# Kernel tuning notes

Hardware: AMD Instinct MI355X
Metric: run time of the kernel (lower is better)

The kernel has to match this reference:

```python
import jax, jax.numpy as jnp
import numpy as np

B, T, Q, K, H = 8, 128, 64, 64, 4  # batch, agents, q_dim, kv_dim, heads; neighbors n = T-1


def setup_inputs() -> dict:
    key = jax.random.key(0)
    ks = jax.random.split(key, 9)
    s = 0.05
    return {
        "q_x": jax.random.normal(ks[0], (B, T, Q), dtype=jnp.float32),
        "kv_x": jax.random.normal(ks[1], (B, T, T - 1, K), dtype=jnp.float32),
        # nn.Linear weights stored (out_features, in_features), y = x @ W.T + b
        "Wk": jax.random.normal(ks[2], (H * K, K), dtype=jnp.float32) * s,      # tokeys (no bias)
        "Wq": jax.random.normal(ks[3], (H * K, Q), dtype=jnp.float32) * s,      # toqueries (no bias)
        "Wv": jax.random.normal(ks[4], (H * K, K + Q), dtype=jnp.float32) * s,  # tovalues
        "bv": jax.random.normal(ks[5], (H * K,), dtype=jnp.float32) * s,
        "bias": jax.random.uniform(ks[6], (K,), dtype=jnp.float32, minval=-0.1, maxval=0.1),
        "ws": jax.random.normal(ks[7], (K,), dtype=jnp.float32) * s,            # score_proj weight (1, K) -> (K,)
        "bs": jax.random.normal(ks[8], (), dtype=jnp.float32) * s,              # score_proj bias
    }


def reference(q_x, kv_x, Wk, Wq, Wv, bv, bias, ws, bs):
    b, t, n, k = kv_x.shape            # n = t - 1 neighbors
    q = q_x.shape[-1]
    h = Wk.shape[0] // k
    # key / query projections
    keys = jnp.einsum('btnk,ok->btno', kv_x, Wk).reshape(b, t, n, h, k)
    queries = jnp.einsum('btq,oq->bto', q_x, Wq).reshape(b, t, 1, h, k)
    # additive (Bahdanau) score: linear(tanh(keys + queries + bias)) -> scalar per (b,t,n,h)
    score = jnp.einsum('btnhk,k->btnh', jnp.tanh(keys + queries + bias), ws) + bs
    # values from concat(kv, broadcast query features)
    q_exp = jnp.broadcast_to(q_x[:, :, None, :], (b, t, n, q))
    value_input = jnp.concatenate([kv_x, q_exp], axis=-1)      # (b,t,n,k+q)
    values = (jnp.einsum('btnc,oc->btno', value_input, Wv) + bv).reshape(b, t, n, h, k)
    # softmax over neighbors, weighted sum of values
    w = jax.nn.softmax(score, axis=2)                          # (b,t,n,h)
    x = jnp.einsum('btnh,btnhk->bthk', w, values).reshape(b, t, h * k)
    return x
```

## Files before the change

kernel.cpp:

```cpp
#include <hip/hip_runtime.h>
#include <hip/hip_bf16.h>

#define NB 127
#define SCALE 2.885390081777927f

typedef __attribute__((ext_vector_type(8))) short bf16x8;
typedef __attribute__((ext_vector_type(4))) float f32x4;

#define WKP_S  0
#define WVP_S  16384
#define WQP_S  32768
#define WVQP_S 49152
#define WS_NEEDED ((size_t)(4 * 16384 * 2))

__device__ __forceinline__ short bfs(float f) {
  __hip_bfloat16 h = __float2bfloat16(f);
  return __builtin_bit_cast(short, h);
}
__device__ __forceinline__ unsigned packbf2(float a, float b) {
  unsigned lo = (unsigned short)bfs(a);
  unsigned hi = (unsigned short)bfs(b);
  return lo | (hi << 16);
}
__device__ __forceinline__ bf16x8 gath_s(const float* __restrict__ p, float s) {
  float4 a = *(const float4*)p;
  float4 b = *(const float4*)(p + 4);
  bf16x8 f;
  f[0] = bfs(a.x * s); f[1] = bfs(a.y * s); f[2] = bfs(a.z * s); f[3] = bfs(a.w * s);
  f[4] = bfs(b.x * s); f[5] = bfs(b.y * s); f[6] = bfs(b.z * s); f[7] = bfs(b.w * s);
  return f;
}

__global__ __launch_bounds__(256, 2) void
pack_kernel(const float* __restrict__ Wk, const float* __restrict__ Wq,
            const float* __restrict__ Wv, short* __restrict__ dstall)
{
  const int blk = blockIdx.x;
  const int tid = threadIdx.x;
  const int m = blk >> 4, sub = blk & 15;
  const float* src; int stride, off, dsto; float scl;
  if (m == 0)      { src = Wk; stride = 64;  off = 0;  dsto = WKP_S;  scl = SCALE; }
  else if (m == 1) { src = Wv; stride = 128; off = 0;  dsto = WVP_S;  scl = 1.f; }
  else if (m == 2) { src = Wq; stride = 64;  off = 0;  dsto = WQP_S;  scl = SCALE; }
  else             { src = Wv; stride = 128; off = 64; dsto = WVQP_S; scl = 1.f; }
  short* dst = dstall + dsto;
  int i4 = sub * 256 + tid;
  int o = i4 >> 4, c4 = i4 & 15;
  float4 v = ((const float4*)(src + o * stride + off))[c4];
  int k0 = c4 * 4;
  int kt = k0 >> 5, gg = (k0 & 31) >> 3, j0 = k0 & 7;
  int head = o >> 6, nt = (o >> 4) & 3, ol = o & 15;
  int di = ((((head * 4 + nt) * 2 + kt) * 64) + gg * 16 + ol) * 8 + j0;
  *(uint2*)(dst + di) = make_uint2(packbf2(v.x * scl, v.y * scl),
                                   packbf2(v.z * scl, v.w * scl));
}

template <int PREP>
__global__ __launch_bounds__(256, 4) void
rnn_attn_kernel(const float* __restrict__ q_x, const float* __restrict__ kv_x,
                const float* __restrict__ Wk, const float* __restrict__ Wq,
                const float* __restrict__ Wv, const float* __restrict__ bv,
                const float* __restrict__ bias, const float* __restrict__ wsc,
                const short* __restrict__ pack, float* __restrict__ out)
{
  __shared__ __align__(16) unsigned char Atile[128 * 128];
  __shared__ float scs[4][128];
  __shared__ float4 qv_lds[4][4][4];

  const int tid = threadIdx.x;
  const int bt = blockIdx.x;
  const int lane = tid & 63;
  const int head = tid >> 6;
  const int l15 = lane & 15;
  const int g = lane >> 4;

  const float* kv = kv_x + (size_t)bt * (NB * 64);
  #pragma unroll
  for (int i = 0; i < 8; ++i) {
    int idx = i * 256 + tid;
    int row = idx >> 4, c = idx & 15;
    float4 v = (row < NB) ? ((const float4*)kv)[idx] : make_float4(0.f, 0.f, 0.f, 0.f);
    int byte = (row << 7) + (c << 3);
    byte ^= ((row & 7) << 4);
    *(uint2*)(&Atile[byte]) = make_uint2(packbf2(v.x, v.y), packbf2(v.z, v.w));
  }

  f32x4 qq[4];
  {
    bf16x8 qf0 = gath_s(q_x + bt * 64 + g * 8, 1.f);
    bf16x8 qf1 = gath_s(q_x + bt * 64 + 32 + g * 8, 1.f);
    #pragma unroll
    for (int nt = 0; nt < 4; ++nt) {
      bf16x8 wv0, wv1;
      if (PREP) {
        const bf16x8* pv = (const bf16x8*)(pack + WVQP_S);
        wv0 = pv[((head * 4 + nt) * 2 + 0) * 64 + lane];
        wv1 = pv[((head * 4 + nt) * 2 + 1) * 64 + lane];
      } else {
        int o = head * 64 + nt * 16 + l15;
        wv0 = gath_s(Wv + o * 128 + 64 + g * 8, 1.f);
        wv1 = gath_s(Wv + o * 128 + 64 + 32 + g * 8, 1.f);
      }
      float4 bv4 = ((const float4*)(bv + head * 64))[nt * 4 + g];
      f32x4 b = (f32x4){bv4.x, bv4.y, bv4.z, bv4.w};
      b = __builtin_amdgcn_mfma_f32_16x16x32_bf16(wv0, qf0, b, 0, 0, 0);
      b = __builtin_amdgcn_mfma_f32_16x16x32_bf16(wv1, qf1, b, 0, 0, 0);
      if (l15 == 0) qv_lds[head][nt][g] = make_float4(b[0], b[1], b[2], b[3]);
    }
    #pragma unroll
    for (int nt = 0; nt < 4; ++nt) {
      bf16x8 wq0, wq1;
      if (PREP) {
        const bf16x8* pw = (const bf16x8*)(pack + WQP_S);
        wq0 = pw[((head * 4 + nt) * 2 + 0) * 64 + lane];
        wq1 = pw[((head * 4 + nt) * 2 + 1) * 64 + lane];
      } else {
        int o = head * 64 + nt * 16 + l15;
        wq0 = gath_s(Wq + o * 64 + g * 8, SCALE);
        wq1 = gath_s(Wq + o * 64 + 32 + g * 8, SCALE);
      }
      float4 bs4 = ((const float4*)bias)[nt * 4 + g];
      f32x4 a = (f32x4){bs4.x * SCALE, bs4.y * SCALE, bs4.z * SCALE, bs4.w * SCALE};
      a = __builtin_amdgcn_mfma_f32_16x16x32_bf16(wq0, qf0, a, 0, 0, 0);
      a = __builtin_amdgcn_mfma_f32_16x16x32_bf16(wq1, qf1, a, 0, 0, 0);
      qq[nt] = a;
    }
  }

  __syncthreads();

  #pragma unroll
  for (int h = 0; h < 2; ++h) {
    bf16x8 b00, b01, b10, b11;
    if (PREP) {
      const bf16x8* pw = (const bf16x8*)(pack + WKP_S);
      b00 = pw[((head * 4 + 2 * h + 0) * 2 + 0) * 64 + lane];
      b01 = pw[((head * 4 + 2 * h + 0) * 2 + 1) * 64 + lane];
      b10 = pw[((head * 4 + 2 * h + 1) * 2 + 0) * 64 + lane];
      b11 = pw[((head * 4 + 2 * h + 1) * 2 + 1) * 64 + lane];
    } else {
      int o0 = head * 64 + (2 * h) * 16 + l15;
      b00 = gath_s(Wk + o0 * 64 + g * 8, SCALE);
      b01 = gath_s(Wk + o0 * 64 + 32 + g * 8, SCALE);
      b10 = gath_s(Wk + (o0 + 16) * 64 + g * 8, SCALE);
      b11 = gath_s(Wk + (o0 + 16) * 64 + 32 + g * 8, SCALE);
    }
    float4 ta = ((const float4*)wsc)[(2 * h) * 4 + g];
    float4 tb = ((const float4*)wsc)[(2 * h + 1) * 4 + g];
    f32x4 wsa = (f32x4){-2.f * ta.x, -2.f * ta.y, -2.f * ta.z, -2.f * ta.w};
    f32x4 wsb = (f32x4){-2.f * tb.x, -2.f * tb.y, -2.f * tb.z, -2.f * tb.w};
    f32x4 qa = qq[2 * h], qb = qq[2 * h + 1];

    #pragma unroll 1
    for (int mt = 0; mt < 8; ++mt) {
      int row = mt * 16 + l15;
      int byte0 = (row << 7) + g * 16;
      int swz = (l15 & 7) << 4;
      bf16x8 a0 = *(const bf16x8*)(&Atile[byte0 ^ swz]);
      bf16x8 a1 = *(const bf16x8*)(&Atile[(byte0 + 64) ^ swz]);
      float p = 0.f;
      f32x4 acc = qa;
      acc = __builtin_amdgcn_mfma_f32_16x16x32_bf16(b00, a0, acc, 0, 0, 0);
      acc = __builtin_amdgcn_mfma_f32_16x16x32_bf16(b01, a1, acc, 0, 0, 0);
      #pragma unroll
      for (int r = 0; r < 4; ++r)
        p = fmaf(wsa[r], __builtin_amdgcn_rcpf(__builtin_amdgcn_exp2f(acc[r]) + 1.f), p);
      f32x4 acc2 = qb;
      acc2 = __builtin_amdgcn_mfma_f32_16x16x32_bf16(b10, a0, acc2, 0, 0, 0);
      acc2 = __builtin_amdgcn_mfma_f32_16x16x32_bf16(b11, a1, acc2, 0, 0, 0);
      #pragma unroll
      for (int r = 0; r < 4; ++r)
        p = fmaf(wsb[r], __builtin_amdgcn_rcpf(__builtin_amdgcn_exp2f(acc2[r]) + 1.f), p);
      p += __shfl_xor(p, 16);
      p += __shfl_xor(p, 32);
      if (g == 0) {
        int idx = mt * 16 + l15;
        scs[head][idx] = h ? (scs[head][idx] + p) : p;
      }
    }
  }

  {
    float s0 = scs[head][l15 + 0],  s1 = scs[head][l15 + 16];
    float s2 = scs[head][l15 + 32], s3 = scs[head][l15 + 48];
    float s4 = scs[head][l15 + 64], s5 = scs[head][l15 + 80];
    float s6 = scs[head][l15 + 96], s7 = scs[head][l15 + 112];
    if (l15 == 15) s7 = -3.0e38f;
    float m = fmaxf(fmaxf(fmaxf(s0, s1), fmaxf(s2, s3)),
                    fmaxf(fmaxf(s4, s5), fmaxf(s6, s7)));
    #pragma unroll
    for (int d = 1; d < 16; d <<= 1) m = fmaxf(m, __shfl_xor(m, d));
    float e0 = __expf(s0 - m), e1 = __expf(s1 - m), e2 = __expf(s2 - m), e3 = __expf(s3 - m);
    float e4 = __expf(s4 - m), e5 = __expf(s5 - m), e6 = __expf(s6 - m), e7 = __expf(s7 - m);
    float sum = ((e0 + e1) + (e2 + e3)) + ((e4 + e5) + (e6 + e7));
    #pragma unroll
    for (int d = 1; d < 16; d <<= 1) sum += __shfl_xor(sum, d);
    float inv = __builtin_amdgcn_rcpf(sum);
    if (g == 0) {
      scs[head][l15 + 0]  = e0 * inv; scs[head][l15 + 16] = e1 * inv;
      scs[head][l15 + 32] = e2 * inv; scs[head][l15 + 48] = e3 * inv;
      scs[head][l15 + 64] = e4 * inv; scs[head][l15 + 80] = e5 * inv;
      scs[head][l15 + 96] = e6 * inv; scs[head][l15 + 112] = e7 * inv;
    }
  }

  #pragma unroll
  for (int h = 0; h < 2; ++h) {
    bf16x8 w00, w01, w10, w11;
    if (PREP) {
      const bf16x8* pw = (const bf16x8*)(pack + WVP_S);
      w00 = pw[((head * 4 + 2 * h + 0) * 2 + 0) * 64 + lane];
      w01 = pw[((head * 4 + 2 * h + 0) * 2 + 1) * 64 + lane];
      w10 = pw[((head * 4 + 2 * h + 1) * 2 + 0) * 64 + lane];
      w11 = pw[((head * 4 + 2 * h + 1) * 2 + 1) * 64 + lane];
    } else {
      int o0 = head * 64 + (2 * h) * 16 + l15;
      w00 = gath_s(Wv + o0 * 128 + g * 8, 1.f);
      w01 = gath_s(Wv + o0 * 128 + 32 + g * 8, 1.f);
      w10 = gath_s(Wv + (o0 + 16) * 128 + g * 8, 1.f);
      w11 = gath_s(Wv + (o0 + 16) * 128 + 32 + g * 8, 1.f);
    }
    f32x4 c0 = (f32x4){0.f, 0.f, 0.f, 0.f};
    f32x4 c1 = (f32x4){0.f, 0.f, 0.f, 0.f};
    #pragma unroll 1
    for (int mt = 0; mt < 8; ++mt) {
      int row = mt * 16 + l15;
      int byte0 = (row << 7) + g * 16;
      int swz = (l15 & 7) << 4;
      bf16x8 a0 = *(const bf16x8*)(&Atile[byte0 ^ swz]);
      bf16x8 a1 = *(const bf16x8*)(&Atile[(byte0 + 64) ^ swz]);
      float w = scs[head][mt * 16 + l15];
      f32x4 v = (f32x4){0.f, 0.f, 0.f, 0.f};
      v = __builtin_amdgcn_mfma_f32_16x16x32_bf16(w00, a0, v, 0, 0, 0);
      v = __builtin_amdgcn_mfma_f32_16x16x32_bf16(w01, a1, v, 0, 0, 0);
      #pragma unroll
      for (int r = 0; r < 4; ++r) c0[r] = fmaf(v[r], w, c0[r]);
      f32x4 v2 = (f32x4){0.f, 0.f, 0.f, 0.f};
      v2 = __builtin_amdgcn_mfma_f32_16x16x32_bf16(w10, a0, v2, 0, 0, 0);
      v2 = __builtin_amdgcn_mfma_f32_16x16x32_bf16(w11, a1, v2, 0, 0, 0);
      #pragma unroll
      for (int r = 0; r < 4; ++r) c1[r] = fmaf(v2[r], w, c1[r]);
    }
    #pragma unroll
    for (int d = 1; d < 16; d <<= 1) {
      #pragma unroll
      for (int r = 0; r < 4; ++r) {
        c0[r] += __shfl_xor(c0[r], d);
        c1[r] += __shfl_xor(c1[r], d);
      }
    }
    if (l15 == 0) {
      float4 qv4 = qv_lds[head][2 * h][g];
      float4 o4 = make_float4(c0[0] + qv4.x, c0[1] + qv4.y, c0[2] + qv4.z, c0[3] + qv4.w);
      ((float4*)out)[bt * 64 + head * 16 + (2 * h) * 4 + g] = o4;
      float4 qv5 = qv_lds[head][2 * h + 1][g];
      float4 o5 = make_float4(c1[0] + qv5.x, c1[1] + qv5.y, c1[2] + qv5.z, c1[3] + qv5.w);
      ((float4*)out)[bt * 64 + head * 16 + (2 * h + 1) * 4 + g] = o5;
    }
  }
}

extern "C" void kernel_launch(void* const* d_in, const int* in_sizes, int n_in,
                              void* d_out, int out_size, void* d_ws, size_t ws_size,
                              hipStream_t stream) {
  const float* q_x  = (const float*)d_in[0];
  const float* kv_x = (const float*)d_in[1];
  const float* Wk   = (const float*)d_in[2];
  const float* Wq   = (const float*)d_in[3];
  const float* Wv   = (const float*)d_in[4];
  const float* bv   = (const float*)d_in[5];
  const float* bias = (const float*)d_in[6];
  const float* wsc  = (const float*)d_in[7];
  float* out = (float*)d_out;
  short* pack = (short*)d_ws;

  if (ws_size >= WS_NEEDED) {
    pack_kernel<<<64, 256, 0, stream>>>(Wk, Wq, Wv, pack);
    rnn_attn_kernel<1><<<1024, 256, 0, stream>>>(q_x, kv_x, Wk, Wq, Wv, bv, bias, wsc, pack, out);
  } else {
    rnn_attn_kernel<0><<<1024, 256, 0, stream>>>(q_x, kv_x, Wk, Wq, Wv, bv, bias, wsc, pack, out);
  }
}
```

Measured before the change: 30.90 us.

## Reassociate value projection: softmax-weighted sum of inputs before Wv matmul

```diff
diff --git a/kernel.cpp b/kernel.cpp
--- a/kernel.cpp
+++ b/kernel.cpp
@@ -21,6 +21,10 @@
   unsigned lo = (unsigned short)bfs(a);
   unsigned hi = (unsigned short)bfs(b);
   return lo | (hi << 16);
+}
+__device__ __forceinline__ float b2f(short s) {
+  unsigned u = ((unsigned)(unsigned short)s) << 16;
+  return __builtin_bit_cast(float, u);
 }
 __device__ __forceinline__ bf16x8 gath_s(const float* __restrict__ p, float s) {
   float4 a = *(const float4*)p;
@@ -204,60 +208,55 @@
     }
   }
 
-  #pragma unroll
-  for (int h = 0; h < 2; ++h) {
-    bf16x8 w00, w01, w10, w11;
+  float pvp0[8], pvp1[8];
+  #pragma unroll
+  for (int j = 0; j < 8; ++j) { pvp0[j] = 0.f; pvp1[j] = 0.f; }
+  #pragma unroll 1
+  for (int mt = 0; mt < 8; ++mt) {
+    int row = mt * 16 + l15;
+    int byte0 = (row << 7) + g * 16;
+    int swz = (l15 & 7) << 4;
+    bf16x8 a0 = *(const bf16x8*)(&Atile[byte0 ^ swz]);
+    bf16x8 a1 = *(const bf16x8*)(&Atile[(byte0 + 64) ^ swz]);
+    float w = scs[head][mt * 16 + l15];
+    #pragma unroll
+    for (int j = 0; j < 8; ++j) {
+      pvp0[j] = fmaf(w, b2f(a0[j]), pvp0[j]);
+      pvp1[j] = fmaf(w, b2f(a1[j]), pvp1[j]);
+    }
+  }
+  bf16x8 pa0, pa1;
+  #pragma unroll
+  for (int j = 0; j < 8; ++j) { pa0[j] = bfs(pvp0[j]); pa1[j] = bfs(pvp1[j]); }
+
+  float tt[4];
+  #pragma unroll 2
+  for (int nt = 0; nt < 4; ++nt) {
+    bf16x8 bw0, bw1;
     if (PREP) {
       const bf16x8* pw = (const bf16x8*)(pack + WVP_S);
-      w00 = pw[((head * 4 + 2 * h + 0) * 2 + 0) * 64 + lane];
-      w01 = pw[((head * 4 + 2 * h + 0) * 2 + 1) * 64 + lane];
-      w10 = pw[((head * 4 + 2 * h + 1) * 2 + 0) * 64 + lane];
-      w11 = pw[((head * 4 + 2 * h + 1) * 2 + 1) * 64 + lane];
+      bw0 = pw[((head * 4 + nt) * 2 + 0) * 64 + lane];
+      bw1 = pw[((head * 4 + nt) * 2 + 1) * 64 + lane];
     } else {
-      int o0 = head * 64 + (2 * h) * 16 + l15;
-      w00 = gath_s(Wv + o0 * 128 + g * 8, 1.f);
-      w01 = gath_s(Wv + o0 * 128 + 32 + g * 8, 1.f);
-      w10 = gath_s(Wv + (o0 + 16) * 128 + g * 8, 1.f);
-      w11 = gath_s(Wv + (o0 + 16) * 128 + 32 + g * 8, 1.f);
-    }
-    f32x4 c0 = (f32x4){0.f, 0.f, 0.f, 0.f};
-    f32x4 c1 = (f32x4){0.f, 0.f, 0.f, 0.f};
-    #pragma unroll 1
-    for (int mt = 0; mt < 8; ++mt) {
-      int row = mt * 16 + l15;
-      int byte0 = (row << 7) + g * 16;
-      int swz = (l15 & 7) << 4;
-      bf16x8 a0 = *(const bf16x8*)(&Atile[byte0 ^ swz]);
-      bf16x8 a1 = *(const bf16x8*)(&Atile[(byte0 + 64) ^ swz]);
-      float w = scs[head][mt * 16 + l15];
-      f32x4 v = (f32x4){0.f, 0.f, 0.f, 0.f};
-      v = __builtin_amdgcn_mfma_f32_16x16x32_bf16(w00, a0, v, 0, 0, 0);
-      v = __builtin_amdgcn_mfma_f32_16x16x32_bf16(w01, a1, v, 0, 0, 0);
-      #pragma unroll
-      for (int r = 0; r < 4; ++r) c0[r] = fmaf(v[r], w, c0[r]);
-      f32x4 v2 = (f32x4){0.f, 0.f, 0.f, 0.f};
-      v2 = __builtin_amdgcn_mfma_f32_16x16x32_bf16(w10, a0, v2, 0, 0, 0);
-      v2 = __builtin_amdgcn_mfma_f32_16x16x32_bf16(w11, a1, v2, 0, 0, 0);
-      #pragma unroll
-      for (int r = 0; r < 4; ++r) c1[r] = fmaf(v2[r], w, c1[r]);
-    }
-    #pragma unroll
-    for (int d = 1; d < 16; d <<= 1) {
-      #pragma unroll
-      for (int r = 0; r < 4; ++r) {
-        c0[r] += __shfl_xor(c0[r], d);
-        c1[r] += __shfl_xor(c1[r], d);
-      }
-    }
-    if (l15 == 0) {
-      float4 qv4 = qv_lds[head][2 * h][g];
-      float4 o4 = make_float4(c0[0] + qv4.x, c0[1] + qv4.y, c0[2] + qv4.z, c0[3] + qv4.w);
-      ((float4*)out)[bt * 64 + head * 16 + (2 * h) * 4 + g] = o4;
-      float4 qv5 = qv_lds[head][2 * h + 1][g];
-      float4 o5 = make_float4(c1[0] + qv5.x, c1[1] + qv5.y, c1[2] + qv5.z, c1[3] + qv5.w);
-      ((float4*)out)[bt * 64 + head * 16 + (2 * h + 1) * 4 + g] = o5;
-    }
-  }
+      int o = head * 64 + nt * 16 + l15;
+      bw0 = gath_s(Wv + o * 128 + g * 8, 1.f);
+      bw1 = gath_s(Wv + o * 128 + 32 + g * 8, 1.f);
+    }
+    f32x4 c = (f32x4){0.f, 0.f, 0.f, 0.f};
+    c = __builtin_amdgcn_mfma_f32_16x16x32_bf16(pa0, bw0, c, 0, 0, 0);
+    c = __builtin_amdgcn_mfma_f32_16x16x32_bf16(pa1, bw1, c, 0, 0, 0);
+    float t = (c[0] + c[1]) + (c[2] + c[3]);
+    t += __shfl_xor(t, 16);
+    t += __shfl_xor(t, 32);
+    tt[nt] = t;
+  }
+
+  float v = tt[0];
+  v = (g == 1) ? tt[1] : v;
+  v = (g == 2) ? tt[2] : v;
+  v = (g == 3) ? tt[3] : v;
+  float qv = ((const float*)&qv_lds[head][g][l15 >> 2])[l15 & 3];
+  out[bt * 256 + head * 64 + lane] = v + qv;
 }
 
 extern "C" void kernel_launch(void* const* d_in, const int* in_sizes, int n_in,
```

Result: faster. 29.07 us (-5.9%).
